# Kernel optimization log

Hardware: AMD Instinct MI355X
Metric: run time of the kernel (lower is better)

## Reference

```python
import jax, jax.numpy as jnp
import numpy as np

E = 500_000   # edges
N = 100_000   # nodes
Q = 256       # queries
N_REL = 200
R = 2 * N_REL + 1  # relation table rows (401)
D = 64        # in_dim
A = 64        # attn_dim
O = 64        # out_dim


def setup_inputs() -> dict:
    key = jax.random.key(0)
    ks = jax.random.split(key, 16)
    s = 1.0 / np.sqrt(D)
    # edges columns: [query_idx, head_ent, rel, tail_ent, sub_node, obj_node]
    col_q = jax.random.randint(ks[0], (E, 1), 0, Q)
    col_h = jax.random.randint(ks[1], (E, 1), 0, N)
    col_r = jax.random.randint(ks[2], (E, 1), 0, R)
    col_t = jax.random.randint(ks[3], (E, 1), 0, N)
    col_s = jax.random.randint(ks[4], (E, 1), 0, N)
    col_o = jax.random.randint(ks[5], (E, 1), 0, N)
    edges = jnp.concatenate([col_q, col_h, col_r, col_t, col_s, col_o], axis=1)
    return {
        "q_sub": jax.random.randint(ks[6], (Q,), 0, N),
        "q_emb": jax.random.normal(ks[7], (Q, D), dtype=jnp.float32),
        "rela_embed": jax.random.normal(ks[8], (R, D), dtype=jnp.float32),
        "hidden": jax.random.normal(ks[9], (N, D), dtype=jnp.float32),
        "edges": edges,
        "n_nodes": N,
        "Ws_W": jax.random.normal(ks[10], (A, D), dtype=jnp.float32) * s,
        "Ws_b": jnp.zeros((A,), dtype=jnp.float32),
        "Wr_W": jax.random.normal(ks[11], (A, D), dtype=jnp.float32) * s,
        "Wq_W": jax.random.normal(ks[12], (A, D), dtype=jnp.float32) * s,
        "Wqr_W": jax.random.normal(ks[13], (A, D), dtype=jnp.float32) * s,
        "wa_W": jax.random.normal(ks[14], (1, A), dtype=jnp.float32) * s,
        "wa_b": jnp.zeros((1,), dtype=jnp.float32),
        "Wh_W": jax.random.normal(ks[15], (O, D), dtype=jnp.float32) * s,
    }


def reference(q_sub, q_emb, rela_embed, hidden, edges, n_nodes,
              Ws_W, Ws_b, Wr_W, Wq_W, Wqr_W, wa_W, wa_b, Wh_W):
    # sample_flag == 0 path of GNNLayer.forward (use_lama_rel == 1, act = identity)
    sub = edges[:, 4]
    rel = edges[:, 2]
    obj = edges[:, 5]
    hs = hidden[sub]            # [E, D] gather
    hr = rela_embed[rel]        # [E, D] gather
    h_qr = q_emb[edges[:, 0]]   # [E, D] gather
    # attention MLP: sigmoid(w_alpha(ReLU(Ws hs + Wr hr + Wq hqr + Wqr (hr*hqr))))
    pre = (jnp.einsum('ed,ad->ea', hs, Ws_W) + Ws_b
           + jnp.einsum('ed,ad->ea', hr, Wr_W)
           + jnp.einsum('ed,ad->ea', h_qr, Wq_W)
           + jnp.einsum('ed,ad->ea', hr * h_qr, Wqr_W))
    alpha = jax.nn.sigmoid(jnp.einsum('ea,oa->eo', jax.nn.relu(pre), wa_W) + wa_b)  # [E,1]
    message = alpha * (hs * hr)                                # [E, D]
    message_agg = jax.ops.segment_sum(message, obj, num_segments=n_nodes)  # [N, D] scatter-sum
    hidden_new = jnp.einsum('nd,od->no', message_agg, Wh_W)    # act = identity
    return hidden_new, alpha
```

## Files before the change

kernel.cpp:

```cpp
#include <hip/hip_runtime.h>
#include <hip/hip_bf16.h>

#define EDGES  500000
#define NNODES 100000
#define QN     256
#define RN     401
#define DD     64
#define AA     64
#define OO     64
#define XSB    1563
#define PB     1604
#define EVB    62500

typedef __attribute__((ext_vector_type(8))) short short8;
typedef __attribute__((ext_vector_type(2))) short short2v;
typedef __attribute__((ext_vector_type(4))) float f32x4;
typedef __attribute__((ext_vector_type(2))) float f32x2;

__device__ inline unsigned short f2bf(float f) {
    union { float f; unsigned int u; } v; v.f = f;
    unsigned int u = v.u;
    u += 0x7FFFu + ((u >> 16) & 1u);
    return (unsigned short)(u >> 16);
}

__device__ inline f32x2 bfpair2f(unsigned int u) {
    union { unsigned int i; float f; } lo, hi;
    lo.i = u << 16;
    hi.i = u & 0xFFFF0000u;
    f32x2 r; r[0] = lo.f; r[1] = hi.f; return r;
}

__device__ inline short8 load8_cvt(const float* __restrict__ p) {
    f32x4 x0 = ((const f32x4*)p)[0];
    f32x4 x1 = ((const f32x4*)p)[1];
    short8 r;
    r[0] = (short)f2bf(x0[0]); r[1] = (short)f2bf(x0[1]);
    r[2] = (short)f2bf(x0[2]); r[3] = (short)f2bf(x0[3]);
    r[4] = (short)f2bf(x1[0]); r[5] = (short)f2bf(x1[1]);
    r[6] = (short)f2bf(x1[2]); r[7] = (short)f2bf(x1[3]);
    return r;
}

__device__ inline short8 load8_cvt_prod(const float* __restrict__ pa,
                                        const float* __restrict__ pb) {
    f32x4 a0 = ((const f32x4*)pa)[0];
    f32x4 a1 = ((const f32x4*)pa)[1];
    f32x4 b0 = ((const f32x4*)pb)[0];
    f32x4 b1 = ((const f32x4*)pb)[1];
    short8 r;
    r[0] = (short)f2bf(a0[0]*b0[0]); r[1] = (short)f2bf(a0[1]*b0[1]);
    r[2] = (short)f2bf(a0[2]*b0[2]); r[3] = (short)f2bf(a0[3]*b0[3]);
    r[4] = (short)f2bf(a1[0]*b1[0]); r[5] = (short)f2bf(a1[1]*b1[1]);
    r[6] = (short)f2bf(a1[2]*b1[2]); r[7] = (short)f2bf(a1[3]*b1[3]);
    return r;
}

__device__ inline void atomic_pk_add_bf16(short* addr, short2v v) {
#if __has_builtin(__builtin_amdgcn_global_atomic_fadd_v2bf16)
    __builtin_amdgcn_global_atomic_fadd_v2bf16(
        (__attribute__((address_space(1))) short2v*)addr, v);
#else
    asm volatile("global_atomic_pk_add_bf16 %0, %1, off"
                 :: "v"(addr), "v"(v) : "memory");
#endif
}

struct Params {
    const float* hidden; const float* Ws_W; const float* q_emb; const float* rela;
    const float* Wq_W;   const float* Wr_W; const float* Wqr_W; const float* Ws_b;
    const int*   edges;  const float* wa_W; const float* wa_b;  const float* Wh_W;
    short* Xs; short* hidden_bf; short* P; short* agg;
    float* out; float* alpha_out;
};

__global__ void k_pre(Params pr) {
    __shared__ short W[AA * 200];
    __shared__ short stage[4][16 * 72];
    int tid = threadIdx.x;
    int wave = tid >> 6, lane = tid & 63;
    int quad = lane >> 4, l15 = lane & 15;
    short* st = stage[wave];

    if (blockIdx.x < XSB) {
        int rowbase_blk = blockIdx.x * 64;
        {
            const short8 z = short8{0,0,0,0,0,0,0,0};
            int base = rowbase_blk * DD + tid * 16;
            int row0 = rowbase_blk + (tid >> 2);
            if (row0 < NNODES) {
                *(short8*)(pr.agg + base) = z;
                *(short8*)(pr.agg + base + 8) = z;
            }
        }
        for (int idx = tid; idx < AA * DD; idx += 256) {
            int a = idx >> 6, d = idx & 63;
            W[a * 72 + d] = (short)f2bf(pr.Ws_W[idx]);
        }
        __syncthreads();
        int rowbase = rowbase_blk + wave * 16;
        int row_a = rowbase + l15;
        f32x4 acc[4];
        for (int t = 0; t < 4; ++t) { acc[t][0]=acc[t][1]=acc[t][2]=acc[t][3]=0.f; }
#pragma unroll
        for (int ks = 0; ks < 2; ++ks) {
            int ka = ks * 32 + quad * 8;
            short8 afrag;
            if (row_a < NNODES) {
                afrag = load8_cvt(pr.hidden + (size_t)row_a * DD + ka);
                *(short8*)(pr.hidden_bf + (size_t)row_a * DD + ka) = afrag;
            } else {
                afrag = short8{0,0,0,0,0,0,0,0};
            }
#pragma unroll
            for (int t = 0; t < 4; ++t) {
                short8 bfrag = *(const short8*)&W[(t * 16 + l15) * 72 + ka];
                acc[t] = __builtin_amdgcn_mfma_f32_16x16x32_bf16(afrag, bfrag, acc[t], 0, 0, 0);
            }
        }
#pragma unroll
        for (int t = 0; t < 4; ++t)
#pragma unroll
            for (int r = 0; r < 4; ++r)
                st[(quad * 4 + r) * 72 + t * 16 + l15] = (short)f2bf(acc[t][r]);
        asm volatile("s_waitcnt lgkmcnt(0)" ::: "memory");
#pragma unroll
        for (int i = 0; i < 2; ++i) {
            int rr = i * 8 + (lane >> 3);
            int cc = (lane & 7) * 8;
            int grow = rowbase + rr;
            if (grow < NNODES) {
                short8 v = *(short8*)&st[rr * 72 + cc];
                *(short8*)&pr.Xs[(size_t)grow * AA + cc] = v;
            }
        }
    } else {
        int pb = blockIdx.x - XSB;
        for (int idx = tid; idx < AA * 192; idx += 256) {
            int a = idx / 192, k = idx - a * 192;
            float v = (k < 64) ? pr.Wq_W[a * 64 + k]
                    : (k < 128) ? pr.Wr_W[a * 64 + (k - 64)]
                                : pr.Wqr_W[a * 64 + (k - 128)];
            W[a * 200 + k] = (short)f2bf(v);
        }
        __syncthreads();
        int pairbase = pb * 64 + wave * 16;
        int mypair = pairbase + l15;
        int q = mypair / RN;
        int r = mypair - q * RN;
        const float* hq = pr.q_emb + (size_t)q * DD;
        const float* hr = pr.rela  + (size_t)r * DD;
        f32x4 acc[4];
#pragma unroll
        for (int t = 0; t < 4; ++t) {
            float b = pr.Ws_b[t * 16 + l15];
            acc[t][0] = acc[t][1] = acc[t][2] = acc[t][3] = b;
        }
#pragma unroll
        for (int ks = 0; ks < 6; ++ks) {
            int ka = ks * 32 + quad * 8;
            short8 afrag;
            if (ka < 64)       afrag = load8_cvt(hq + ka);
            else if (ka < 128) afrag = load8_cvt(hr + (ka - 64));
            else               afrag = load8_cvt_prod(hq + (ka - 128), hr + (ka - 128));
#pragma unroll
            for (int t = 0; t < 4; ++t) {
                short8 bfrag = *(const short8*)&W[(t * 16 + l15) * 200 + ka];
                acc[t] = __builtin_amdgcn_mfma_f32_16x16x32_bf16(afrag, bfrag, acc[t], 0, 0, 0);
            }
        }
#pragma unroll
        for (int t = 0; t < 4; ++t)
#pragma unroll
            for (int rg = 0; rg < 4; ++rg)
                st[(quad * 4 + rg) * 72 + t * 16 + l15] = (short)f2bf(acc[t][rg]);
        asm volatile("s_waitcnt lgkmcnt(0)" ::: "memory");
#pragma unroll
        for (int i = 0; i < 2; ++i) {
            int rr = i * 8 + (lane >> 3);
            int cc = (lane & 7) * 8;
            int prow = pairbase + rr;
            short8 v = *(short8*)&st[rr * 72 + cc];
            *(short8*)&pr.P[(size_t)prow * AA + cc] = v;
        }
    }
}

__global__ void k_edge(Params pr) {
    int tid  = threadIdx.x;
    int wave = tid >> 6, lane = tid & 63;
    int l32  = lane & 31;
    int half = lane >> 5;
    size_t e = (size_t)blockIdx.x * 8 + wave * 2 + half;

    const int* ep = pr.edges + e * 6;
    int q = ep[0];
    int r = ep[2];
    int2 so = *(const int2*)&ep[4];
    int sub = so.x, obj = so.y;

    int c2 = 2 * l32;
    unsigned xs_u = *(const unsigned*)&pr.Xs[(size_t)sub * AA + c2];
    unsigned pp_u = *(const unsigned*)&pr.P[((size_t)q * RN + r) * AA + c2];
    f32x2 xs = bfpair2f(xs_u);
    f32x2 pp = bfpair2f(pp_u);
    f32x2 wa = *(const f32x2*)&pr.wa_W[c2];

    float v = fmaxf(xs[0] + pp[0], 0.f) * wa[0]
            + fmaxf(xs[1] + pp[1], 0.f) * wa[1];
#pragma unroll
    for (int off = 16; off > 0; off >>= 1) v += __shfl_xor(v, off, 64);
    float alpha = 1.f / (1.f + __expf(-(v + pr.wa_b[0])));
    if (l32 == 0) pr.alpha_out[e] = alpha;

    unsigned hs_u = *(const unsigned*)&pr.hidden_bf[(size_t)sub * DD + c2];
    f32x2 hs = bfpair2f(hs_u);
    f32x2 hr = *(const f32x2*)&pr.rela[(size_t)r * DD + c2];
    short2v m;
    m[0] = (short)f2bf(alpha * hs[0] * hr[0]);
    m[1] = (short)f2bf(alpha * hs[1] * hr[1]);
    atomic_pk_add_bf16(pr.agg + (size_t)obj * DD + c2, m);
}

__global__ void k_out(Params pr) {
    __shared__ short W[OO * 72];
    __shared__ float stF[4][16 * 68];
    int tid = threadIdx.x;
    for (int idx = tid; idx < OO * DD; idx += 256) {
        int o = idx >> 6, d = idx & 63;
        W[o * 72 + d] = (short)f2bf(pr.Wh_W[idx]);
    }
    __syncthreads();
    int wave = tid >> 6, lane = tid & 63;
    int quad = lane >> 4, l15 = lane & 15;
    int rowbase = blockIdx.x * 64 + wave * 16;
    int row_a = rowbase + l15;
    float* st = stF[wave];

    f32x4 acc[4];
    for (int t = 0; t < 4; ++t) { acc[t][0]=acc[t][1]=acc[t][2]=acc[t][3]=0.f; }
#pragma unroll
    for (int ks = 0; ks < 2; ++ks) {
        int ka = ks * 32 + quad * 8;
        short8 afrag;
        if (row_a < NNODES) afrag = *(const short8*)(pr.agg + (size_t)row_a * DD + ka);
        else                afrag = short8{0,0,0,0,0,0,0,0};
#pragma unroll
        for (int t = 0; t < 4; ++t) {
            short8 bfrag = *(const short8*)&W[(t * 16 + l15) * 72 + ka];
            acc[t] = __builtin_amdgcn_mfma_f32_16x16x32_bf16(afrag, bfrag, acc[t], 0, 0, 0);
        }
    }
#pragma unroll
    for (int t = 0; t < 4; ++t)
#pragma unroll
        for (int r = 0; r < 4; ++r)
            st[(quad * 4 + r) * 68 + t * 16 + l15] = acc[t][r];
    asm volatile("s_waitcnt lgkmcnt(0)" ::: "memory");
#pragma unroll
    for (int i = 0; i < 4; ++i) {
        int rr = i * 4 + (lane >> 4);
        int cc = (lane & 15) * 4;
        int grow = rowbase + rr;
        if (grow < NNODES) {
            f32x4 v = *(f32x4*)&st[rr * 68 + cc];
            *(f32x4*)&pr.out[(size_t)grow * OO + cc] = v;
        }
    }
}

extern "C" void kernel_launch(void* const* d_in, const int* in_sizes, int n_in,
                              void* d_out, int out_size, void* d_ws, size_t ws_size,
                              hipStream_t stream) {
    Params pr;
    pr.q_emb  = (const float*)d_in[1];
    pr.rela   = (const float*)d_in[2];
    pr.hidden = (const float*)d_in[3];
    pr.edges  = (const int*)d_in[4];
    pr.Ws_W   = (const float*)d_in[6];
    pr.Ws_b   = (const float*)d_in[7];
    pr.Wr_W   = (const float*)d_in[8];
    pr.Wq_W   = (const float*)d_in[9];
    pr.Wqr_W  = (const float*)d_in[10];
    pr.wa_W   = (const float*)d_in[11];
    pr.wa_b   = (const float*)d_in[12];
    pr.Wh_W   = (const float*)d_in[13];

    short* Xs        = (short*)d_ws;
    short* P         = Xs + (size_t)NNODES * AA;
    short* hidden_bf = P + (size_t)QN * RN * AA;
    short* agg       = hidden_bf + (size_t)NNODES * DD;
    pr.Xs = Xs; pr.P = P; pr.hidden_bf = hidden_bf; pr.agg = agg;

    pr.out       = (float*)d_out;
    pr.alpha_out = pr.out + (size_t)NNODES * OO;

    k_pre<<<XSB + PB, 256, 0, stream>>>(pr);
    k_edge<<<EVB, 256, 0, stream>>>(pr);
    k_out<<<XSB, 256, 0, stream>>>(pr);
}
```

Before: 204.2 us.

## Process 8 edges per wave with 16-byte vector loads in edge kernel

The edge kernel now maps 8 lanes per edge instead of 32, so each wave handles 8 edges. Each lane loads 16-byte vectors of Xs, P, hidden and relation rows. Edge indices are fetched with one coalesced load per wave and broadcast by shuffles. The attention reduction shortens to three shuffle steps, and the grid shrinks by a factor of four. Weight staging in the other kernels now converts pairs of floats per thread. The aim is fewer instructions and fewer memory transactions per edge; each lane still issues four packed bf16 atomics.

Result: slower. 349.1 us (+71.0%).

```diff
diff --git a/kernel.cpp b/kernel.cpp
--- a/kernel.cpp
+++ b/kernel.cpp
@@ -10,7 +10,7 @@
 #define OO     64
 #define XSB    1563
 #define PB     1604
-#define EVB    62500
+#define EB     15625
 
 typedef __attribute__((ext_vector_type(8))) short short8;
 typedef __attribute__((ext_vector_type(2))) short short2v;
@@ -22,6 +22,10 @@
     unsigned int u = v.u;
     u += 0x7FFFu + ((u >> 16) & 1u);
     return (unsigned short)(u >> 16);
+}
+
+__device__ inline unsigned pack2bf(float lo, float hi) {
+    return (unsigned)f2bf(lo) | ((unsigned)f2bf(hi) << 16);
 }
 
 __device__ inline f32x2 bfpair2f(unsigned int u) {
@@ -66,6 +70,10 @@
 #endif
 }
 
+__device__ inline void atomic_pk_add_bf16_u(short* addr, unsigned v) {
+    atomic_pk_add_bf16(addr, __builtin_bit_cast(short2v, v));
+}
+
 struct Params {
     const float* hidden; const float* Ws_W; const float* q_emb; const float* rela;
     const float* Wq_W;   const float* Wr_W; const float* Wqr_W; const float* Ws_b;
@@ -93,9 +101,10 @@
                 *(short8*)(pr.agg + base + 8) = z;
             }
         }
-        for (int idx = tid; idx < AA * DD; idx += 256) {
-            int a = idx >> 6, d = idx & 63;
-            W[a * 72 + d] = (short)f2bf(pr.Ws_W[idx]);
+        for (int idx = tid; idx < (AA * DD) / 2; idx += 256) {
+            int a = idx >> 5, d2 = (idx & 31) * 2;
+            f32x2 x = *(const f32x2*)(pr.Ws_W + a * 64 + d2);
+            *reinterpret_cast<unsigned*>(&W[a * 72 + d2]) = pack2bf(x[0], x[1]);
         }
         __syncthreads();
         int rowbase = rowbase_blk + wave * 16;
@@ -136,12 +145,15 @@
         }
     } else {
         int pb = blockIdx.x - XSB;
-        for (int idx = tid; idx < AA * 192; idx += 256) {
-            int a = idx / 192, k = idx - a * 192;
-            float v = (k < 64) ? pr.Wq_W[a * 64 + k]
-                    : (k < 128) ? pr.Wr_W[a * 64 + (k - 64)]
-                                : pr.Wqr_W[a * 64 + (k - 128)];
-            W[a * 200 + k] = (short)f2bf(v);
+#pragma unroll
+        for (int m = 0; m < 3; ++m) {
+            const float* src = (m == 0) ? pr.Wq_W : (m == 1) ? pr.Wr_W : pr.Wqr_W;
+            for (int idx = tid; idx < (AA * DD) / 2; idx += 256) {
+                int a = idx >> 5, d2 = (idx & 31) * 2;
+                f32x2 x = *(const f32x2*)(src + a * 64 + d2);
+                *reinterpret_cast<unsigned*>(&W[a * 200 + m * 64 + d2]) =
+                    pack2bf(x[0], x[1]);
+            }
         }
         __syncthreads();
         int pairbase = pb * 64 + wave * 16;
@@ -188,47 +200,72 @@
 
 __global__ void k_edge(Params pr) {
     int tid  = threadIdx.x;
-    int wave = tid >> 6, lane = tid & 63;
-    int l32  = lane & 31;
-    int half = lane >> 5;
-    size_t e = (size_t)blockIdx.x * 8 + wave * 2 + half;
-
-    const int* ep = pr.edges + e * 6;
-    int q = ep[0];
-    int r = ep[2];
-    int2 so = *(const int2*)&ep[4];
-    int sub = so.x, obj = so.y;
-
-    int c2 = 2 * l32;
-    unsigned xs_u = *(const unsigned*)&pr.Xs[(size_t)sub * AA + c2];
-    unsigned pp_u = *(const unsigned*)&pr.P[((size_t)q * RN + r) * AA + c2];
-    f32x2 xs = bfpair2f(xs_u);
-    f32x2 pp = bfpair2f(pp_u);
-    f32x2 wa = *(const f32x2*)&pr.wa_W[c2];
-
-    float v = fmaxf(xs[0] + pp[0], 0.f) * wa[0]
-            + fmaxf(xs[1] + pp[1], 0.f) * wa[1];
-#pragma unroll
-    for (int off = 16; off > 0; off >>= 1) v += __shfl_xor(v, off, 64);
+    int lane = tid & 63;
+    int l8   = tid & 7;
+    int g    = lane >> 3;
+    int wave = tid >> 6;
+    size_t ewave = (size_t)blockIdx.x * 32 + wave * 8;
+    size_t e = ewave + g;
+
+    const int* ebase = pr.edges + ewave * 6;
+    int eval = (lane < 48) ? ebase[lane] : 0;
+    int q   = __shfl(eval, g * 6 + 0, 64);
+    int r   = __shfl(eval, g * 6 + 2, 64);
+    int sub = __shfl(eval, g * 6 + 4, 64);
+    int obj = __shfl(eval, g * 6 + 5, 64);
+    int qr  = q * RN + r;
+    int c8  = l8 * 8;
+
+    short8 xs8 = *(const short8*)(pr.Xs + (size_t)sub * AA + c8);
+    short8 pp8 = *(const short8*)(pr.P  + (size_t)qr  * AA + c8);
+    f32x4 waA = *(const f32x4*)(pr.wa_W + c8);
+    f32x4 waB = *(const f32x4*)(pr.wa_W + c8 + 4);
+
+    typedef __attribute__((ext_vector_type(4))) unsigned int uint4v;
+    uint4v xu = __builtin_bit_cast(uint4v, xs8);
+    uint4v pu = __builtin_bit_cast(uint4v, pp8);
+    f32x2 acc2; acc2[0] = 0.f; acc2[1] = 0.f;
+#pragma unroll
+    for (int j = 0; j < 4; ++j) {
+        f32x2 a = bfpair2f(xu[j]);
+        f32x2 b = bfpair2f(pu[j]);
+        f32x2 s = a + b;
+        float wlo = (j < 2) ? waA[2*j]     : waB[2*j - 4];
+        float whi = (j < 2) ? waA[2*j + 1] : waB[2*j - 3];
+        acc2[0] += fmaxf(s[0], 0.f) * wlo;
+        acc2[1] += fmaxf(s[1], 0.f) * whi;
+    }
+    float v = acc2[0] + acc2[1];
+    v += __shfl_xor(v, 1, 64);
+    v += __shfl_xor(v, 2, 64);
+    v += __shfl_xor(v, 4, 64);
     float alpha = 1.f / (1.f + __expf(-(v + pr.wa_b[0])));
-    if (l32 == 0) pr.alpha_out[e] = alpha;
-
-    unsigned hs_u = *(const unsigned*)&pr.hidden_bf[(size_t)sub * DD + c2];
-    f32x2 hs = bfpair2f(hs_u);
-    f32x2 hr = *(const f32x2*)&pr.rela[(size_t)r * DD + c2];
-    short2v m;
-    m[0] = (short)f2bf(alpha * hs[0] * hr[0]);
-    m[1] = (short)f2bf(alpha * hs[1] * hr[1]);
-    atomic_pk_add_bf16(pr.agg + (size_t)obj * DD + c2, m);
+    if (l8 == 0) pr.alpha_out[e] = alpha;
+
+    short8 hs8 = *(const short8*)(pr.hidden_bf + (size_t)sub * DD + c8);
+    f32x4 hrA = *(const f32x4*)(pr.rela + (size_t)r * DD + c8);
+    f32x4 hrB = *(const f32x4*)(pr.rela + (size_t)r * DD + c8 + 4);
+    uint4v hu = __builtin_bit_cast(uint4v, hs8);
+    short* aggp = pr.agg + (size_t)obj * DD + c8;
+#pragma unroll
+    for (int j = 0; j < 4; ++j) {
+        f32x2 h = bfpair2f(hu[j]);
+        float hrlo = (j < 2) ? hrA[2*j]     : hrB[2*j - 4];
+        float hrhi = (j < 2) ? hrA[2*j + 1] : hrB[2*j - 3];
+        float m0 = alpha * h[0] * hrlo;
+        float m1 = alpha * h[1] * hrhi;
+        atomic_pk_add_bf16_u(aggp + 2 * j, pack2bf(m0, m1));
+    }
 }
 
 __global__ void k_out(Params pr) {
     __shared__ short W[OO * 72];
     __shared__ float stF[4][16 * 68];
     int tid = threadIdx.x;
-    for (int idx = tid; idx < OO * DD; idx += 256) {
-        int o = idx >> 6, d = idx & 63;
-        W[o * 72 + d] = (short)f2bf(pr.Wh_W[idx]);
+    for (int idx = tid; idx < (OO * DD) / 2; idx += 256) {
+        int o = idx >> 5, d2 = (idx & 31) * 2;
+        f32x2 x = *(const f32x2*)(pr.Wh_W + o * 64 + d2);
+        *reinterpret_cast<unsigned*>(&W[o * 72 + d2]) = pack2bf(x[0], x[1]);
     }
     __syncthreads();
     int wave = tid >> 6, lane = tid & 63;
@@ -296,6 +333,6 @@
     pr.alpha_out = pr.out + (size_t)NNODES * OO;
 
     k_pre<<<XSB + PB, 256, 0, stream>>>(pr);
-    k_edge<<<EVB, 256, 0, stream>>>(pr);
+    k_edge<<<EB, 256, 0, stream>>>(pr);
     k_out<<<XSB, 256, 0, stream>>>(pr);
 }
```
